# Kernel optimization log

Measured on AMD Instinct MI355X. Metric: run time of the kernel, lower is better.

Reference implementation:

```python
import jax, jax.numpy as jnp
import numpy as np

IN_FEATURES = 256
EMBED = 512
HEADS = 8
HEAD_DIM = EMBED // HEADS
BLOCKS = 2
FFN = 2048
CLASSES = 1000
NWIRES = 8
BATCH = 8
SEQ = 2048


def _posenc(seq, dim, dtype):
    pos = jnp.arange(seq, dtype=jnp.float32)[:, None]
    div = jnp.exp(jnp.arange(0, dim, 2, dtype=jnp.float32) * (-jnp.log(10000.0) / dim))
    pe = jnp.zeros((seq, dim), dtype=jnp.float32)
    pe = pe.at[:, 0::2].set(jnp.sin(pos * div))
    pe = pe.at[:, 1::2].set(jnp.cos(pos * div))
    return pe.astype(dtype)


def _layer_norm(x, g, b, eps=1e-5):
    mu = jnp.mean(x, axis=-1, keepdims=True)
    var = jnp.var(x, axis=-1, keepdims=True)
    return (x - mu) * jax.lax.rsqrt(var + eps) * g + b


def setup_inputs() -> dict:
    key = jax.random.key(0)
    ks = jax.random.split(key, 20)
    s = 0.02
    inp = {
        'x': jax.random.normal(ks[0], (BATCH, SEQ, IN_FEATURES), dtype=jnp.float32),
        'Wi': jax.random.normal(ks[1], (EMBED, IN_FEATURES), dtype=jnp.float32) * s,
        'bi': jnp.zeros((EMBED,), dtype=jnp.float32),
        'theta_a': jax.random.normal(ks[2], (BLOCKS, NWIRES), dtype=jnp.float32),
        'Wproj': jax.random.normal(ks[3], (BLOCKS, EMBED, NWIRES), dtype=jnp.float32) * s,
        'Wq': jax.random.normal(ks[4], (BLOCKS, EMBED, EMBED), dtype=jnp.float32) * s,
        'Wk': jax.random.normal(ks[5], (BLOCKS, EMBED, EMBED), dtype=jnp.float32) * s,
        'Wv': jax.random.normal(ks[6], (BLOCKS, EMBED, EMBED), dtype=jnp.float32) * s,
        'Wo': jax.random.normal(ks[7], (BLOCKS, EMBED, EMBED), dtype=jnp.float32) * s,
        'g1': jnp.ones((BLOCKS, EMBED), dtype=jnp.float32),
        'b1': jnp.zeros((BLOCKS, EMBED), dtype=jnp.float32),
        'phi': jax.random.normal(ks[8], (BLOCKS, NWIRES), dtype=jnp.float32),
        'W1': jax.random.normal(ks[9], (BLOCKS, FFN, NWIRES), dtype=jnp.float32) * s,
        'W2': jax.random.normal(ks[10], (BLOCKS, EMBED, FFN), dtype=jnp.float32) * s,
        'g2': jnp.ones((BLOCKS, EMBED), dtype=jnp.float32),
        'b2': jnp.zeros((BLOCKS, EMBED), dtype=jnp.float32),
        'Wc': jax.random.normal(ks[11], (CLASSES, EMBED), dtype=jnp.float32) * s,
        'bc': jnp.zeros((CLASSES,), dtype=jnp.float32),
    }
    return inp


def reference(x, Wi, bi, theta_a, Wproj, Wq, Wk, Wv, Wo, g1, b1, phi, W1, W2, g2, b2, Wc, bc):
    b, s, _ = x.shape
    h = jnp.einsum('bsf,ef->bse', x, Wi) + bi          # input_proj
    h = h + _posenc(s, EMBED, h.dtype)[None]           # positional encoding
    scale = 1.0 / np.sqrt(HEAD_DIM)
    for l in range(BLOCKS):
        # --- quantum attention sublayer ---
        # RX encode first NWIRES features + trainable RX per wire -> <Z> = cos(x + theta)
        q_out = jnp.cos(h[..., :NWIRES] + theta_a[l])  # [b,s,nw]
        x_q = jnp.einsum('bsw,ew->bse', q_out, Wproj[l])
        q = jnp.einsum('bse,fe->bsf', x_q, Wq[l]).reshape(b, s, HEADS, HEAD_DIM).transpose(0, 2, 1, 3)
        k = jnp.einsum('bse,fe->bsf', x_q, Wk[l]).reshape(b, s, HEADS, HEAD_DIM).transpose(0, 2, 1, 3)
        v = jnp.einsum('bse,fe->bsf', x_q, Wv[l]).reshape(b, s, HEADS, HEAD_DIM).transpose(0, 2, 1, 3)
        scores = jnp.einsum('bhqd,bhkd->bhqk', q, k) * scale
        attn = jax.nn.softmax(scores, axis=-1)
        out = jnp.einsum('bhqk,bhkd->bhqd', attn, v)
        out = out.transpose(0, 2, 1, 3).reshape(b, s, EMBED)
        attn_out = jnp.einsum('bse,fe->bsf', out, Wo[l])
        h = _layer_norm(h + attn_out, g1[l], b1[l])
        # --- quantum feed-forward sublayer ---
        # RY encode + trainable RY per wire -> <Z> = cos(x + phi)
        qf = jnp.cos(h[..., :NWIRES] + phi[l])         # [b,s,nw]
        f = jnp.einsum('bsw,fw->bsf', qf, W1[l])       # nw -> ffn
        f = jnp.einsum('bsf,ef->bse', jax.nn.relu(f), W2[l])
        h = _layer_norm(h + f, g2[l], b2[l])
    pooled = jnp.mean(h, axis=1)                        # [b, embed]
    logits = jnp.einsum('be,ce->bc', pooled, Wc) + bc
    return logits
```

## Files before the change

kernel.cpp:

```cpp
#include <hip/hip_runtime.h>
#include <hip/hip_bf16.h>
#include <math.h>

#define B_   8
#define S_   2048
#define T_   (B_*S_)
#define FIN  256
#define E_   512
#define H_   8
#define D_   64
#define FFN_ 2048
#define NC_  1000
#define NW_  8

typedef __attribute__((ext_vector_type(8))) short short8;
typedef __attribute__((ext_vector_type(4))) short short4v;
typedef __attribute__((ext_vector_type(4))) float f32x4;
typedef __attribute__((ext_vector_type(2))) unsigned int uint2v;
typedef __attribute__((ext_vector_type(4))) unsigned int uint4v;

__device__ __forceinline__ unsigned short f2bf(float f) {
    __hip_bfloat16 h = __float2bfloat16(f);
    return __builtin_bit_cast(unsigned short, h);
}
__device__ __forceinline__ float bf2f(unsigned short u) {
    return __builtin_bit_cast(float, (unsigned int)u << 16);
}

__device__ __forceinline__ unsigned cvtpk_bf16(float lo, float hi) {
    unsigned r;
    asm("v_cvt_pk_bf16_f32 %0, %1, %2" : "=v"(r) : "v"(lo), "v"(hi));
    return r;
}

#if defined(__has_builtin)
#if __has_builtin(__builtin_amdgcn_permlane32_swap) && __has_builtin(__builtin_amdgcn_permlane16_swap)
#define HAVE_PLSWAP 1
#endif
#endif

__device__ __forceinline__ void lswap32(unsigned &a, unsigned &b) {
#if defined(HAVE_PLSWAP)
    uint2v t = __builtin_amdgcn_permlane32_swap(a, b, false, false);
    a = t[0]; b = t[1];
#else
    unsigned as = (unsigned)__shfl_xor((int)a, 32);
    unsigned bs = (unsigned)__shfl_xor((int)b, 32);
    bool hi = (threadIdx.x & 32) != 0;
    unsigned na = hi ? bs : a;
    unsigned nb = hi ? b  : as;
    a = na; b = nb;
#endif
}
__device__ __forceinline__ void lswap16(unsigned &a, unsigned &b) {
#if defined(HAVE_PLSWAP)
    uint2v t = __builtin_amdgcn_permlane16_swap(a, b, false, false);
    a = t[0]; b = t[1];
#else
    unsigned as = (unsigned)__shfl_xor((int)a, 16);
    unsigned bs = (unsigned)__shfl_xor((int)b, 16);
    bool hi = (threadIdx.x & 16) != 0;
    unsigned na = hi ? bs : a;
    unsigned nb = hi ? b  : as;
    a = na; b = nb;
#endif
}

__device__ __forceinline__ void gld16(void* l, const void* g) {
    __builtin_amdgcn_global_load_lds(
        (const __attribute__((address_space(1))) unsigned int*)g,
        (__attribute__((address_space(3))) unsigned int*)l,
        16, 0, 0);
}

#if defined(__has_builtin)
#if __has_builtin(__builtin_amdgcn_mfma_f32_16x16x16bf16_1k)
#define HAVE_MFMA16 1
#endif
#endif

__device__ __forceinline__ f32x4 mfma16(short4v a, short4v b, f32x4 c) {
#ifdef HAVE_MFMA16
    return __builtin_amdgcn_mfma_f32_16x16x16bf16_1k(a, b, c, 0, 0, 0);
#else
    short8 a8 = {a[0], a[1], a[2], a[3], 0, 0, 0, 0};
    short8 b8 = {b[0], b[1], b[2], b[3], 0, 0, 0, 0};
    return __builtin_amdgcn_mfma_f32_16x16x32_bf16(a8, b8, c, 0, 0, 0);
#endif
}

__global__ __launch_bounds__(256)
void cvt_all(const float* __restrict__ x,  const float* __restrict__ Wi,
             const float* __restrict__ Wo, const float* __restrict__ W2,
             const float* __restrict__ W1,
             unsigned short* xb, unsigned short* Wib,
             unsigned short* Wob, unsigned short* W2b, unsigned short* W1b)
{
    int g = blockIdx.x*256 + threadIdx.x;
    const float* s; unsigned short* d; int o;
    if      (g < 1048576) { s = x;  d = xb;  o = g; }
    else if (g < 1081344) { s = Wi; d = Wib; o = g - 1048576; }
    else if (g < 1212416) { s = Wo; d = Wob; o = g - 1081344; }
    else if (g < 1736704) { s = W2; d = W2b; o = g - 1212416; }
    else                  { s = W1; d = W1b; o = g - 1736704; }
    float4 vv = ((const float4*)s)[o];
    ushort4 u;
    u.x = f2bf(vv.x); u.y = f2bf(vv.y); u.z = f2bf(vv.z); u.w = f2bf(vv.w);
    ((ushort4*)d)[o] = u;
}

__global__ __launch_bounds__(64)
void weff_kernel(const float* __restrict__ Wq, const float* __restrict__ Wk,
                 const float* __restrict__ Wv, const float* __restrict__ Wproj,
                 unsigned short* __restrict__ Weff)
{
    const int f = blockIdx.x, l = blockIdx.y, which = blockIdx.z;
    const int lane = threadIdx.x;
    const float* W = (which == 0 ? Wq : which == 1 ? Wk : Wv)
                     + (size_t)l*E_*E_ + (size_t)f*E_;
    const float* P = Wproj + (size_t)l*E_*NW_;
    const int wv = lane & 7;
    float s = 0.f;
    for (int e = (lane >> 3)*64; e < (lane >> 3)*64 + 64; e++)
        s += W[e] * P[e*NW_ + wv];
    #pragma unroll
    for (int off = 8; off < 64; off <<= 1) s += __shfl_xor(s, off);
    const float scale = (which == 0) ? 0.18033688011112042f : 1.f;
    if (lane < 8)
        Weff[((size_t)(which*2 + l)*E_ + f)*NW_ + lane] = f2bf(s * scale);
}

__global__ __launch_bounds__(256)
void qkv_small(const unsigned short* __restrict__ h, const float* __restrict__ theta,
               const unsigned short* __restrict__ Wq_e,
               const unsigned short* __restrict__ Wk_e,
               const unsigned short* __restrict__ Wv_e,
               unsigned short* __restrict__ qo, unsigned short* __restrict__ ko,
               unsigned short* __restrict__ vT)
{
    const int tid = threadIdx.x;
    const int t0 = blockIdx.x * 32;
    __shared__ float cs[32][8];
    {
        int tl = tid >> 3, wv2 = tid & 7;
        cs[tl][wv2] = cosf(bf2f(h[(size_t)(t0 + tl)*E_ + wv2]) + theta[wv2]);
    }
    __syncthreads();
    const int f = tid * 2;
    float wq[16], wk[16], wv_[16];
    #pragma unroll
    for (int i = 0; i < 16; i++) {
        wq[i]  = bf2f(Wq_e[(size_t)f*NW_ + i]);
        wk[i]  = bf2f(Wk_e[(size_t)f*NW_ + i]);
        wv_[i] = bf2f(Wv_e[(size_t)f*NW_ + i]);
    }
    unsigned int v0p[16] __attribute__((aligned(16)));
    unsigned int v1p[16] __attribute__((aligned(16)));
    for (int t = 0; t < 32; t++) {
        float4 c01 = *(const float4*)&cs[t][0];
        float4 c23 = *(const float4*)&cs[t][4];
        float c[8] = {c01.x,c01.y,c01.z,c01.w,c23.x,c23.y,c23.z,c23.w};
        float q0=0,q1=0,k0=0,k1=0,v0=0,v1=0;
        #pragma unroll
        for (int i = 0; i < 8; i++) {
            q0 += c[i]*wq[i];  q1 += c[i]*wq[8+i];
            k0 += c[i]*wk[i];  k1 += c[i]*wk[8+i];
            v0 += c[i]*wv_[i]; v1 += c[i]*wv_[8+i];
        }
        size_t base = (size_t)(t0 + t)*E_ + f;
        ushort2 uq; uq.x = f2bf(q0); uq.y = f2bf(q1);
        ushort2 uk; uk.x = f2bf(k0); uk.y = f2bf(k1);
        *(ushort2*)&qo[base] = uq;
        *(ushort2*)&ko[base] = uk;
        unsigned int b0 = f2bf(v0), b1 = f2bf(v1);
        if (t & 1) { v0p[t>>1] |= b0 << 16; v1p[t>>1] |= b1 << 16; }
        else       { v0p[t>>1]  = b0;       v1p[t>>1]  = b1; }
    }
    const int bb = t0 >> 11, s0 = t0 & (S_ - 1);
    const int head = f >> 6, d = f & 63;
    unsigned short* r0 = vT + ((size_t)(bb*H_ + head)*64 + d)*S_ + s0;
    #pragma unroll
    for (int c = 0; c < 4; c++) *(float4*)(r0 + c*8) = *(float4*)&v0p[c*4];
    r0 += S_;
    #pragma unroll
    for (int c = 0; c < 4; c++) *(float4*)(r0 + c*8) = *(float4*)&v1p[c*4];
}

template<int TC_BF16, int MODE>
__global__ __launch_bounds__(256)
void gemm_mfma(const unsigned short* __restrict__ A,
               const unsigned short* __restrict__ Bm,
               void* __restrict__ Cv, int M, int N, int K,
               float scale, const float* __restrict__ bias)
{
    __shared__ char Lraw[32768];
    unsigned short* Al = (unsigned short*)Lraw;
    unsigned short* Bl = (unsigned short*)(Lraw + 16384);
    float* Ot = (float*)Lraw;

    const int tid  = threadIdx.x;
    const int lane = tid & 63;
    const int w    = tid >> 6;
    const int wx   = w & 1, wy = w >> 1;
    int bx, by;
    {
        int nx = gridDim.x;
        int bid = blockIdx.y * nx + blockIdx.x;
        int rpx = gridDim.y >> 3;
        int xcd = bid & 7, idx = bid >> 3;
        by = xcd * rpx + idx / nx;
        bx = idx % nx;
    }
    const int rowBase = by * 128;
    const int colBase = bx * 128;
    const int l15  = lane & 15;
    const int quad = lane >> 4;
    const int srow = lane >> 2;
    const int gch  = (lane & 3) ^ ((srow >> 1) & 3);
    const int swz  = (l15 >> 1) & 3;

    f32x4 acc[4][4] = {};

    #pragma unroll
    for (int it = 0; it < 2; it++) {
        int rb = it*64 + w*16;
        gld16(&Al[rb*32], A  + (size_t)(rowBase + rb + srow)*K + gch*8);
        gld16(&Bl[rb*32], Bm + (size_t)(colBase + rb + srow)*K + gch*8);
    }

    for (int k0 = 0; k0 < K; k0 += 32) {
        const int cur = (k0 >> 5) & 1;
        __syncthreads();
        if (k0 + 32 < K) {
            #pragma unroll
            for (int it = 0; it < 2; it++) {
                int rb = it*64 + w*16;
                gld16(&Al[(1-cur)*4096 + rb*32], A  + (size_t)(rowBase + rb + srow)*K + k0 + 32 + gch*8);
                gld16(&Bl[(1-cur)*4096 + rb*32], Bm + (size_t)(colBase + rb + srow)*K + k0 + 32 + gch*8);
            }
        }
        short8 af[4], bfr[4];
        #pragma unroll
        for (int mi = 0; mi < 4; mi++)
            af[mi] = *(const short8*)&Al[cur*4096 + (wy*64 + mi*16 + l15)*32 + ((quad ^ swz) << 3)];
        #pragma unroll
        for (int ni = 0; ni < 4; ni++)
            bfr[ni] = *(const short8*)&Bl[cur*4096 + (wx*64 + ni*16 + l15)*32 + ((quad ^ swz) << 3)];
        #pragma unroll
        for (int mi = 0; mi < 4; mi++)
            #pragma unroll
            for (int ni = 0; ni < 4; ni++)
                acc[mi][ni] = __builtin_amdgcn_mfma_f32_16x16x32_bf16(
                    af[mi], bfr[ni], acc[mi][ni], 0, 0, 0);
    }

    #pragma unroll
    for (int mi = 0; mi < 4; mi++) {
        __syncthreads();
        #pragma unroll
        for (int ni = 0; ni < 4; ni++) {
            #pragma unroll
            for (int r = 0; r < 4; r++) {
                float v = acc[mi][ni][r] * scale;
                if (MODE == 1) {
                    int row = rowBase + wy*64 + mi*16 + quad*4 + r;
                    int col = colBase + wx*64 + ni*16 + l15;
                    int s = row & (S_ - 1);
                    float freq = __expf(-0.017988946039244957f * (float)(col & ~1));
                    float ang = (float)s * freq;
                    v += bias[col] + ((col & 1) ? cosf(ang) : sinf(ang));
                }
                Ot[(wy*16 + quad*4 + r)*132 + wx*64 + ni*16 + l15] = v;
            }
        }
        __syncthreads();
        {
            int rl = tid >> 3, c0 = (tid & 7) * 16;
            int grow = rowBase + (rl >> 4)*64 + mi*16 + (rl & 15);
            float vv[16];
            #pragma unroll
            for (int j = 0; j < 4; j++)
                *(float4*)&vv[j*4] = *(const float4*)&Ot[rl*132 + c0 + j*4];
            if (TC_BF16) {
                unsigned short u[16] __attribute__((aligned(16)));
                #pragma unroll
                for (int i = 0; i < 16; i++) u[i] = f2bf(vv[i]);
                unsigned short* dst = (unsigned short*)Cv + (size_t)grow*N + colBase + c0;
                *(float4*)dst       = *(float4*)&u[0];
                *(float4*)(dst + 8) = *(float4*)&u[8];
            } else {
                float* dst = (float*)Cv + (size_t)grow*N + colBase + c0;
                #pragma unroll
                for (int j = 0; j < 4; j++)
                    *(float4*)(dst + j*4) = *(const float4*)&vv[j*4];
            }
        }
    }
}

__global__ __launch_bounds__(256)
void gemm_w2f(const unsigned short* __restrict__ h, const float* __restrict__ phi,
              const unsigned short* __restrict__ W1b,
              const unsigned short* __restrict__ W2b,
              unsigned short* __restrict__ tmp)
{
    __shared__ char Lraw[17408];
    unsigned short* Wl = (unsigned short*)Lraw;
    float* Ot = (float*)Lraw;

    const int tid  = threadIdx.x;
    const int lane = tid & 63;
    const int w    = tid >> 6;
    const int tx   = w & 1, ty = w >> 1;
    const int l15  = lane & 15;
    const int quad = lane >> 4;
    const int srow = lane >> 2;
    const int gch  = (lane & 3) ^ ((srow >> 1) & 3);
    const int swz  = (l15 >> 1) & 3;

    const int bid = blockIdx.x;
    const int xcd = bid & 7;
    const int eb  = xcd >> 1;
    const int tb  = (xcd & 1) * 64 + (bid >> 3);
    const int tBase = tb * 128;
    const int eBase = eb * 128;

    short4v cosfr[4];
    #pragma unroll
    for (int nt = 0; nt < 4; nt++) {
        short4v c = {0,0,0,0};
        if (quad < 2) {
            int tok = tBase + ty*64 + nt*16 + l15;
            #pragma unroll
            for (int i = 0; i < 4; i++) {
                int wv = quad*4 + i;
                c[i] = (short)f2bf(cosf(bf2f(h[(size_t)tok*E_ + wv]) + phi[wv]));
            }
        }
        cosfr[nt] = c;
    }

    #pragma unroll
    for (int it = 0; it < 2; it++) {
        int rb = w*32 + it*16;
        gld16(&Wl[rb*32], W2b + (size_t)(eBase + rb + srow)*FFN_ + gch*8);
    }
    short4v w1f[2] = {{0,0,0,0},{0,0,0,0}};
    #pragma unroll
    for (int jb = 0; jb < 2; jb++)
        if (quad < 2)
            w1f[jb] = *(const short4v*)&W1b[(size_t)(jb*16 + l15)*NW_ + quad*4];

    f32x4 acc[4][4] = {};
    const f32x4 fzero = {0.f, 0.f, 0.f, 0.f};

    for (int k0 = 0; k0 < FFN_; k0 += 32) {
        const int cur = (k0 >> 5) & 1;
        __syncthreads();
        if (k0 + 32 < FFN_) {
            #pragma unroll
            for (int it = 0; it < 2; it++) {
                int rb = w*32 + it*16;
                gld16(&Wl[(1-cur)*4096 + rb*32],
                      W2b + (size_t)(eBase + rb + srow)*FFN_ + k0 + 32 + gch*8);
            }
        }
        unsigned Pm[4][4];
        #pragma unroll
        for (int nt = 0; nt < 4; nt++) {
            #pragma unroll
            for (int jb = 0; jb < 2; jb++) {
                f32x4 c = mfma16(w1f[jb], cosfr[nt], fzero);
                Pm[nt][jb*2]   = cvtpk_bf16(fmaxf(c[0], 0.f), fmaxf(c[1], 0.f));
                Pm[nt][jb*2+1] = cvtpk_bf16(fmaxf(c[2], 0.f), fmaxf(c[3], 0.f));
            }
            lswap32(Pm[nt][0], Pm[nt][2]); lswap32(Pm[nt][1], Pm[nt][3]);
            lswap16(Pm[nt][0], Pm[nt][2]); lswap16(Pm[nt][1], Pm[nt][3]);
        }
        short8 pfr[4];
        #pragma unroll
        for (int nt = 0; nt < 4; nt++) {
            uint4v u = { Pm[nt][0], Pm[nt][1], Pm[nt][2], Pm[nt][3] };
            pfr[nt] = __builtin_bit_cast(short8, u);
        }
        if (k0 + 32 < FFN_) {
            #pragma unroll
            for (int jb = 0; jb < 2; jb++)
                if (quad < 2)
                    w1f[jb] = *(const short4v*)&W1b[(size_t)(k0 + 32 + jb*16 + l15)*NW_ + quad*4];
        }
        #pragma unroll
        for (int et = 0; et < 4; et++) {
            short8 wf = *(const short8*)&Wl[cur*4096 + (tx*64 + et*16 + l15)*32
                                             + ((quad ^ swz) << 3)];
            #pragma unroll
            for (int nt = 0; nt < 4; nt++)
                acc[et][nt] = __builtin_amdgcn_mfma_f32_16x16x32_bf16(
                    wf, pfr[nt], acc[et][nt], 0, 0, 0);
        }
    }

    #pragma unroll
    for (int et = 0; et < 4; et++) {
        __syncthreads();
        #pragma unroll
        for (int nt = 0; nt < 4; nt++)
            #pragma unroll
            for (int r = 0; r < 4; r++)
                Ot[(ty*64 + nt*16 + l15)*33 + tx*16 + quad*4 + r] = acc[et][nt][r];
        __syncthreads();
        int token = tid >> 1, half = tid & 1;
        unsigned short u[16] __attribute__((aligned(16)));
        #pragma unroll
        for (int i = 0; i < 16; i++) u[i] = f2bf(Ot[token*33 + half*16 + i]);
        unsigned short* dst = tmp + (size_t)(tBase + token)*E_ + eBase + half*64 + et*16;
        *(float4*)dst       = *(float4*)&u[0];
        *(float4*)(dst + 8) = *(float4*)&u[8];
    }
}

__global__ __launch_bounds__(256)
void flash_attn(const unsigned short* __restrict__ q,
                const unsigned short* __restrict__ k,
                const unsigned short* __restrict__ vT,
                unsigned short* __restrict__ o)
{
    __shared__ unsigned short L[17168];
    unsigned short* Ks = L;
    unsigned short* Vt = L + 8192;
    float* Ot = (float*)L;

    const int tid  = threadIdx.x;
    const int lane = tid & 63;
    const int w    = tid >> 6;
    const int l15  = lane & 15;
    const int quad = lane >> 4;
    const int bid  = blockIdx.x;
    const int xcd  = bid & 7;
    const int rest = bid >> 3;
    const int combo = xcd * 8 + (rest >> 4);
    const int qt = rest & 15;
    const int hh = combo & 7;
    const int bb = combo >> 3;
    const size_t qrow0 = (size_t)bb*S_ + (size_t)qt*128;
    const unsigned short* qp  = q  + qrow0*E_ + hh*64;
    const unsigned short* kp  = k  + ((size_t)bb*S_)*E_ + hh*64;
    const unsigned short* vtp = vT + (size_t)(bb*H_ + hh)*64*S_;

    const int srow8 = lane >> 3;
    const int gch8  = (lane & 7) ^ srow8;
    const int sql   = l15 & 7;

    #pragma unroll
    for (int it = 0; it < 4; it++) {
        int rb = it*32 + w*8;
        gld16(&L[rb*64], qp + (size_t)(rb + srow8)*E_ + gch8*8);
    }
    __syncthreads();
    short8 qfr[2][2];
    #pragma unroll
    for (int mi = 0; mi < 2; mi++)
        #pragma unroll
        for (int kc = 0; kc < 2; kc++)
            qfr[mi][kc] = *(const short8*)&L[(w*32 + mi*16 + l15)*64
                                             + (((kc*4 + quad) ^ sql) << 3)];
    __syncthreads();

    #pragma unroll
    for (int it = 0; it < 2; it++) {
        int rb = it*32 + w*8;
        gld16(&Ks[rb*64], kp  + (size_t)(rb + srow8)*E_ + gch8*8);
        gld16(&Vt[rb*64], vtp + (size_t)(rb + srow8)*S_ + gch8*8);
    }

    const short8 ones8 = {(short)0x3F80, (short)0x3F80, (short)0x3F80, (short)0x3F80,
                          (short)0x3F80, (short)0x3F80, (short)0x3F80, (short)0x3F80};
    f32x4 O[2][4] = {};
    f32x4 Ol[2]   = {};

    for (int kt = 0; kt < S_/64; kt++) {
        const int cur = kt & 1;
        __syncthreads();
        if (kt + 1 < S_/64) {
            #pragma unroll
            for (int it = 0; it < 2; it++) {
                int rb = it*32 + w*8;
                gld16(&Ks[(1-cur)*4096 + rb*64],
                      kp  + (size_t)((kt+1)*64 + rb + srow8)*E_ + gch8*8);
                gld16(&Vt[(1-cur)*4096 + rb*64],
                      vtp + (size_t)(rb + srow8)*S_ + (kt+1)*64 + gch8*8);
            }
        }
        f32x4 Sc[2][4] = {};
        #pragma unroll
        for (int kc = 0; kc < 2; kc++)
            #pragma unroll
            for (int nt = 0; nt < 4; nt++) {
                short8 kf = *(const short8*)&Ks[cur*4096 + (nt*16 + l15)*64
                                                 + (((kc*4 + quad) ^ sql) << 3)];
                Sc[0][nt] = __builtin_amdgcn_mfma_f32_16x16x32_bf16(kf, qfr[0][kc], Sc[0][nt], 0, 0, 0);
                Sc[1][nt] = __builtin_amdgcn_mfma_f32_16x16x32_bf16(kf, qfr[1][kc], Sc[1][nt], 0, 0, 0);
            }
        unsigned Pm[2][8];
        #pragma unroll
        for (int mi = 0; mi < 2; mi++)
            #pragma unroll
            for (int nt = 0; nt < 4; nt++) {
                float e0 = __builtin_amdgcn_exp2f(Sc[mi][nt][0]);
                float e1 = __builtin_amdgcn_exp2f(Sc[mi][nt][1]);
                float e2 = __builtin_amdgcn_exp2f(Sc[mi][nt][2]);
                float e3 = __builtin_amdgcn_exp2f(Sc[mi][nt][3]);
                Pm[mi][nt*2]   = cvtpk_bf16(e0, e1);
                Pm[mi][nt*2+1] = cvtpk_bf16(e2, e3);
            }
        #pragma unroll
        for (int mi = 0; mi < 2; mi++) {
            lswap32(Pm[mi][0], Pm[mi][2]); lswap32(Pm[mi][1], Pm[mi][3]);
            lswap32(Pm[mi][4], Pm[mi][6]); lswap32(Pm[mi][5], Pm[mi][7]);
            lswap16(Pm[mi][0], Pm[mi][2]); lswap16(Pm[mi][1], Pm[mi][3]);
            lswap16(Pm[mi][4], Pm[mi][6]); lswap16(Pm[mi][5], Pm[mi][7]);
        }
        short8 pf[2][2];
        #pragma unroll
        for (int mi = 0; mi < 2; mi++)
            #pragma unroll
            for (int kb = 0; kb < 2; kb++) {
                uint4v u = { Pm[mi][kb*4], Pm[mi][kb*4+1], Pm[mi][kb*4+2], Pm[mi][kb*4+3] };
                pf[mi][kb] = __builtin_bit_cast(short8, u);
                Ol[mi] = __builtin_amdgcn_mfma_f32_16x16x32_bf16(ones8, pf[mi][kb], Ol[mi], 0, 0, 0);
            }
        #pragma unroll
        for (int dt = 0; dt < 4; dt++)
            #pragma unroll
            for (int kb = 0; kb < 2; kb++) {
                short8 vf = *(const short8*)&Vt[cur*4096 + (dt*16 + l15)*64
                                                 + (((kb*4 + quad) ^ sql) << 3)];
                O[0][dt] = __builtin_amdgcn_mfma_f32_16x16x32_bf16(vf, pf[0][kb], O[0][dt], 0, 0, 0);
                O[1][dt] = __builtin_amdgcn_mfma_f32_16x16x32_bf16(vf, pf[1][kb], O[1][dt], 0, 0, 0);
            }
    }

    __syncthreads();
    #pragma unroll
    for (int mi = 0; mi < 2; mi++) {
        float inv = 1.f / Ol[mi][0];
        #pragma unroll
        for (int dt = 0; dt < 4; dt++)
            #pragma unroll
            for (int r = 0; r < 4; r++)
                Ot[(w*32 + mi*16 + l15)*67 + dt*16 + quad*4 + r] = O[mi][dt][r] * inv;
    }
    __syncthreads();
    {
        int row = tid >> 1, half = tid & 1;
        unsigned short u[32] __attribute__((aligned(16)));
        #pragma unroll
        for (int i = 0; i < 32; i++) u[i] = f2bf(Ot[row*67 + half*32 + i]);
        unsigned short* dst = o + (qrow0 + row)*E_ + hh*64 + half*32;
        #pragma unroll
        for (int c = 0; c < 4; c++) *(float4*)(dst + c*8) = *(float4*)&u[c*8];
    }
}

__global__ __launch_bounds__(256)
void add_ln(unsigned short* __restrict__ h, const unsigned short* __restrict__ delta,
            const float* __restrict__ g, const float* __restrict__ b)
{
    const int lane = threadIdx.x & 63;
    const int t = blockIdx.x*4 + (threadIdx.x >> 6);
    const size_t base = (size_t)t*E_ + lane*8;
    uint4 hv = *(const uint4*)&h[base];
    uint4 dv = *(const uint4*)&delta[base];
    float x[8];
    #pragma unroll
    for (int i = 0; i < 4; i++) {
        unsigned hu = ((const unsigned*)&hv)[i], du = ((const unsigned*)&dv)[i];
        x[2*i]   = bf2f((unsigned short)(hu & 0xffff)) + bf2f((unsigned short)(du & 0xffff));
        x[2*i+1] = bf2f((unsigned short)(hu >> 16))    + bf2f((unsigned short)(du >> 16));
    }
    float s = 0.f, sq = 0.f;
    #pragma unroll
    for (int i = 0; i < 8; i++) { s += x[i]; sq += x[i]*x[i]; }
    #pragma unroll
    for (int off = 1; off < 64; off <<= 1) {
        s  += __shfl_xor(s,  off);
        sq += __shfl_xor(sq, off);
    }
    float mu  = s * (1.f/E_);
    float var = sq * (1.f/E_) - mu*mu;
    float rstd = rsqrtf(var + 1e-5f);
    float4 g0 = *(const float4*)&g[lane*8], g1 = *(const float4*)&g[lane*8 + 4];
    float4 b0 = *(const float4*)&b[lane*8], b1 = *(const float4*)&b[lane*8 + 4];
    float gg[8] = {g0.x,g0.y,g0.z,g0.w,g1.x,g1.y,g1.z,g1.w};
    float bb[8] = {b0.x,b0.y,b0.z,b0.w,b1.x,b1.y,b1.z,b1.w};
    uint4 ov;
    #pragma unroll
    for (int i = 0; i < 4; i++) {
        unsigned lo = f2bf((x[2*i]   - mu)*rstd*gg[2*i]   + bb[2*i]);
        unsigned hi = f2bf((x[2*i+1] - mu)*rstd*gg[2*i+1] + bb[2*i+1]);
        ((unsigned*)&ov)[i] = lo | (hi << 16);
    }
    *(uint4*)&h[base] = ov;
}

__global__ __launch_bounds__(256)
void pool_partial(const unsigned short* __restrict__ h, float* __restrict__ part)
{
    const int chunk = blockIdx.x, bb = blockIdx.y, tid = threadIdx.x;
    for (int e = tid; e < E_; e += 256) {
        const unsigned short* p = h + ((size_t)bb*S_ + (size_t)chunk*128)*E_ + e;
        float s = 0.f;
        for (int r = 0; r < 128; r++) s += bf2f(p[(size_t)r*E_]);
        part[(size_t)(bb*16 + chunk)*E_ + e] = s;
    }
}

__global__ __launch_bounds__(256)
void pool_final(const float* __restrict__ part, float* __restrict__ pooled)
{
    const int bb = blockIdx.x, tid = threadIdx.x;
    for (int e = tid; e < E_; e += 256) {
        float s = 0.f;
        #pragma unroll
        for (int c = 0; c < 16; c++) s += part[(size_t)(bb*16 + c)*E_ + e];
        pooled[bb*E_ + e] = s * (1.f/S_);
    }
}

__global__ __launch_bounds__(64)
void classify(const float* __restrict__ pooled, const float* __restrict__ Wc,
              const float* __restrict__ bc, float* __restrict__ out)
{
    const int c = blockIdx.x, bb = blockIdx.y, lane = threadIdx.x;
    const float* p = pooled + bb*E_;
    const float* wc = Wc + (size_t)c*E_;
    float s = 0.f;
    for (int e = lane; e < E_; e += 64) s += p[e]*wc[e];
    #pragma unroll
    for (int off = 1; off < 64; off <<= 1) s += __shfl_xor(s, off);
    if (lane == 0) out[bb*NC_ + c] = s + bc[c];
}

extern "C" void kernel_launch(void* const* d_in, const int* in_sizes, int n_in,
                              void* d_out, int out_size, void* d_ws, size_t ws_size,
                              hipStream_t stream)
{
    const float* x       = (const float*)d_in[0];
    const float* Wi      = (const float*)d_in[1];
    const float* bi      = (const float*)d_in[2];
    const float* theta_a = (const float*)d_in[3];
    const float* Wproj   = (const float*)d_in[4];
    const float* Wq      = (const float*)d_in[5];
    const float* Wk      = (const float*)d_in[6];
    const float* Wv      = (const float*)d_in[7];
    const float* Wo      = (const float*)d_in[8];
    const float* g1      = (const float*)d_in[9];
    const float* b1      = (const float*)d_in[10];
    const float* phi     = (const float*)d_in[11];
    const float* W1      = (const float*)d_in[12];
    const float* W2      = (const float*)d_in[13];
    const float* g2      = (const float*)d_in[14];
    const float* b2      = (const float*)d_in[15];
    const float* Wc      = (const float*)d_in[16];
    const float* bc      = (const float*)d_in[17];
    float* out = (float*)d_out;

    char* ws = (char*)d_ws;
    const size_t MB = 1024u*1024u;
    unsigned short* h      = (unsigned short*)(ws + 0*MB);
    unsigned short* tmp    = (unsigned short*)(ws + 16*MB);
    unsigned short* qb     = (unsigned short*)(ws + 32*MB);
    unsigned short* kb     = (unsigned short*)(ws + 48*MB);
    unsigned short* vT     = (unsigned short*)(ws + 64*MB);
    unsigned short* ao     = (unsigned short*)(ws + 80*MB);
    unsigned short* xb     = (unsigned short*)(ws + 96*MB);
    unsigned short* Wib    = (unsigned short*)(ws + 104*MB);
    unsigned short* Wob    = (unsigned short*)(ws + 105*MB);
    unsigned short* W2b    = (unsigned short*)(ws + 106*MB);
    unsigned short* W1b    = (unsigned short*)(ws + 110*MB);
    unsigned short* Weff   = (unsigned short*)(ws + 111*MB);
    float*          part   = (float*)(ws + 112*MB);
    float*          pooled = (float*)(ws + 112*MB + 512*1024);

    cvt_all<<<6816, 256, 0, stream>>>(x, Wi, Wo, W2, W1, xb, Wib, Wob, W2b, W1b);
    weff_kernel<<<dim3(E_, 2, 3), 64, 0, stream>>>(Wq, Wk, Wv, Wproj, Weff);

    gemm_mfma<1,1><<<dim3(E_/128, T_/128), 256, 0, stream>>>(
        xb, Wib, h, T_, E_, FIN, 1.f, bi);

    for (int l = 0; l < 2; l++) {
        const unsigned short* Wq_e = Weff + (size_t)(0*2 + l)*E_*NW_;
        const unsigned short* Wk_e = Weff + (size_t)(1*2 + l)*E_*NW_;
        const unsigned short* Wv_e = Weff + (size_t)(2*2 + l)*E_*NW_;
        qkv_small<<<T_/32, 256, 0, stream>>>(h, theta_a + l*NW_, Wq_e, Wk_e, Wv_e, qb, kb, vT);
        flash_attn<<<(S_/128)*H_*B_, 256, 0, stream>>>(qb, kb, vT, ao);
        gemm_mfma<1,0><<<dim3(E_/128, T_/128), 256, 0, stream>>>(
            ao, Wob + (size_t)l*E_*E_, tmp, T_, E_, E_, 1.f, nullptr);
        add_ln<<<T_/4, 256, 0, stream>>>(h, tmp, g1 + l*E_, b1 + l*E_);

        gemm_w2f<<<512, 256, 0, stream>>>(h, phi + l*NW_,
                                          W1b + (size_t)l*FFN_*NW_,
                                          W2b + (size_t)l*E_*FFN_, tmp);
        add_ln<<<T_/4, 256, 0, stream>>>(h, tmp, g2 + l*E_, b2 + l*E_);
    }

    pool_partial<<<dim3(16, B_), 256, 0, stream>>>(h, part);
    pool_final<<<B_, 256, 0, stream>>>(part, pooled);
    classify<<<dim3(NC_, B_), 64, 0, stream>>>(pooled, Wc, bc, out);
}
```

Baseline: 638.6 us.

## Exploit rank-8 structure: attention scores via Gram matrix, fold Wv into Wo

```diff
diff --git a/kernel.cpp b/kernel.cpp
--- a/kernel.cpp
+++ b/kernel.cpp
@@ -130,60 +130,80 @@
         Weff[((size_t)(which*2 + l)*E_ + f)*NW_ + lane] = f2bf(s * scale);
 }
 
-__global__ __launch_bounds__(256)
-void qkv_small(const unsigned short* __restrict__ h, const float* __restrict__ theta,
-               const unsigned short* __restrict__ Wq_e,
-               const unsigned short* __restrict__ Wk_e,
-               const unsigned short* __restrict__ Wv_e,
-               unsigned short* __restrict__ qo, unsigned short* __restrict__ ko,
-               unsigned short* __restrict__ vT)
+__global__ __launch_bounds__(64)
+void gram_kernel(const unsigned short* __restrict__ Weff, unsigned short* __restrict__ G)
+{
+    const int hh = blockIdx.x, l = blockIdx.y;
+    const int lane = threadIdx.x;
+    const int w = lane >> 3, wp = lane & 7;
+    const unsigned short* Wq_e = Weff + (size_t)(0*2 + l)*E_*NW_ + (size_t)hh*64*NW_;
+    const unsigned short* Wk_e = Weff + (size_t)(1*2 + l)*E_*NW_ + (size_t)hh*64*NW_;
+    float s = 0.f;
+    for (int d = 0; d < 64; d++)
+        s += bf2f(Wq_e[d*NW_ + w]) * bf2f(Wk_e[d*NW_ + wp]);
+    G[(size_t)(l*8 + hh)*64 + w*8 + wp] = f2bf(s);
+}
+
+__global__ __launch_bounds__(64)
+void wov_kernel(const float* __restrict__ Wo, const unsigned short* __restrict__ Weff,
+                unsigned short* __restrict__ WoV)
+{
+    const int f = blockIdx.x, l = blockIdx.y;
+    const int lane = threadIdx.x;
+    const int hh = lane >> 3, w = lane & 7;
+    const float* wrow = Wo + (size_t)l*E_*E_ + (size_t)f*E_ + hh*64;
+    const unsigned short* Wv_e = Weff + (size_t)(2*2 + l)*E_*NW_ + (size_t)hh*64*NW_;
+    float s = 0.f;
+    for (int d = 0; d < 64; d++)
+        s += wrow[d] * bf2f(Wv_e[d*NW_ + w]);
+    WoV[(size_t)(l*E_ + f)*64 + lane] = f2bf(s);
+}
+
+__global__ __launch_bounds__(256)
+void qc_small(const unsigned short* __restrict__ h, const float* __restrict__ theta,
+              const unsigned short* __restrict__ G,
+              unsigned short* __restrict__ c8, unsigned short* __restrict__ c8T,
+              unsigned short* __restrict__ gkb)
 {
     const int tid = threadIdx.x;
     const int t0 = blockIdx.x * 32;
     __shared__ float cs[32][8];
+    __shared__ float Gs[512];
     {
         int tl = tid >> 3, wv2 = tid & 7;
         cs[tl][wv2] = cosf(bf2f(h[(size_t)(t0 + tl)*E_ + wv2]) + theta[wv2]);
+        Gs[tid]       = bf2f(G[tid]);
+        Gs[tid + 256] = bf2f(G[tid + 256]);
     }
     __syncthreads();
-    const int f = tid * 2;
-    float wq[16], wk[16], wv_[16];
-    #pragma unroll
-    for (int i = 0; i < 16; i++) {
-        wq[i]  = bf2f(Wq_e[(size_t)f*NW_ + i]);
-        wk[i]  = bf2f(Wk_e[(size_t)f*NW_ + i]);
-        wv_[i] = bf2f(Wv_e[(size_t)f*NW_ + i]);
-    }
-    unsigned int v0p[16] __attribute__((aligned(16)));
-    unsigned int v1p[16] __attribute__((aligned(16)));
-    for (int t = 0; t < 32; t++) {
-        float4 c01 = *(const float4*)&cs[t][0];
-        float4 c23 = *(const float4*)&cs[t][4];
-        float c[8] = {c01.x,c01.y,c01.z,c01.w,c23.x,c23.y,c23.z,c23.w};
-        float q0=0,q1=0,k0=0,k1=0,v0=0,v1=0;
-        #pragma unroll
-        for (int i = 0; i < 8; i++) {
-            q0 += c[i]*wq[i];  q1 += c[i]*wq[8+i];
-            k0 += c[i]*wk[i];  k1 += c[i]*wk[8+i];
-            v0 += c[i]*wv_[i]; v1 += c[i]*wv_[8+i];
-        }
-        size_t base = (size_t)(t0 + t)*E_ + f;
-        ushort2 uq; uq.x = f2bf(q0); uq.y = f2bf(q1);
-        ushort2 uk; uk.x = f2bf(k0); uk.y = f2bf(k1);
-        *(ushort2*)&qo[base] = uq;
-        *(ushort2*)&ko[base] = uk;
-        unsigned int b0 = f2bf(v0), b1 = f2bf(v1);
-        if (t & 1) { v0p[t>>1] |= b0 << 16; v1p[t>>1] |= b1 << 16; }
-        else       { v0p[t>>1]  = b0;       v1p[t>>1]  = b1; }
-    }
-    const int bb = t0 >> 11, s0 = t0 & (S_ - 1);
-    const int head = f >> 6, d = f & 63;
-    unsigned short* r0 = vT + ((size_t)(bb*H_ + head)*64 + d)*S_ + s0;
-    #pragma unroll
-    for (int c = 0; c < 4; c++) *(float4*)(r0 + c*8) = *(float4*)&v0p[c*4];
-    r0 += S_;
-    #pragma unroll
-    for (int c = 0; c < 4; c++) *(float4*)(r0 + c*8) = *(float4*)&v1p[c*4];
+    const int tl = tid >> 3, hh = tid & 7;
+    const int bb = (t0 + tl) >> 11, ss = (t0 + tl) & (S_ - 1);
+    float c[8];
+    #pragma unroll
+    for (int i = 0; i < 8; i++) c[i] = cs[tl][i];
+    unsigned short u[8] __attribute__((aligned(16)));
+    #pragma unroll
+    for (int w = 0; w < 8; w++) {
+        float s = 0.f;
+        #pragma unroll
+        for (int wp = 0; wp < 8; wp++) s += Gs[hh*64 + w*8 + wp] * c[wp];
+        u[w] = f2bf(s);
+    }
+    *(float4*)&gkb[((size_t)(bb*H_ + hh)*S_ + ss)*8] = *(float4*)u;
+    if (tid < 32) {
+        unsigned short v[8] __attribute__((aligned(16)));
+        #pragma unroll
+        for (int i = 0; i < 8; i++) v[i] = f2bf(cs[tid][i]);
+        *(float4*)&c8[(size_t)(t0 + tid)*8] = *(float4*)v;
+    } else if (tid < 40) {
+        int w = tid - 32;
+        unsigned short v[32] __attribute__((aligned(16)));
+        #pragma unroll
+        for (int s = 0; s < 32; s++) v[s] = f2bf(cs[s][w]);
+        unsigned short* dst = c8T + ((size_t)(t0 >> 11)*8 + w)*S_ + (t0 & (S_ - 1));
+        #pragma unroll
+        for (int cq = 0; cq < 4; cq++) *(float4*)(dst + cq*8) = *(float4*)&v[cq*8];
+    }
 }
 
 template<int TC_BF16, int MODE>
@@ -420,19 +440,14 @@
 }
 
 __global__ __launch_bounds__(256)
-void flash_attn(const unsigned short* __restrict__ q,
-                const unsigned short* __restrict__ k,
-                const unsigned short* __restrict__ vT,
-                unsigned short* __restrict__ o)
-{
-    __shared__ unsigned short L[17168];
-    unsigned short* Ks = L;
-    unsigned short* Vt = L + 8192;
-    float* Ot = (float*)L;
-
+void flash_q(const unsigned short* __restrict__ c8,
+             const unsigned short* __restrict__ c8T,
+             const unsigned short* __restrict__ gkb,
+             unsigned short* __restrict__ yout)
+{
     const int tid  = threadIdx.x;
     const int lane = tid & 63;
-    const int w    = tid >> 6;
+    const int wv   = tid >> 6;
     const int l15  = lane & 15;
     const int quad = lane >> 4;
     const int bid  = blockIdx.x;
@@ -443,64 +458,29 @@
     const int hh = combo & 7;
     const int bb = combo >> 3;
     const size_t qrow0 = (size_t)bb*S_ + (size_t)qt*128;
-    const unsigned short* qp  = q  + qrow0*E_ + hh*64;
-    const unsigned short* kp  = k  + ((size_t)bb*S_)*E_ + hh*64;
-    const unsigned short* vtp = vT + (size_t)(bb*H_ + hh)*64*S_;
-
-    const int srow8 = lane >> 3;
-    const int gch8  = (lane & 7) ^ srow8;
-    const int sql   = l15 & 7;
-
-    #pragma unroll
-    for (int it = 0; it < 4; it++) {
-        int rb = it*32 + w*8;
-        gld16(&L[rb*64], qp + (size_t)(rb + srow8)*E_ + gch8*8);
-    }
-    __syncthreads();
-    short8 qfr[2][2];
-    #pragma unroll
-    for (int mi = 0; mi < 2; mi++)
-        #pragma unroll
-        for (int kc = 0; kc < 2; kc++)
-            qfr[mi][kc] = *(const short8*)&L[(w*32 + mi*16 + l15)*64
-                                             + (((kc*4 + quad) ^ sql) << 3)];
-    __syncthreads();
-
-    #pragma unroll
-    for (int it = 0; it < 2; it++) {
-        int rb = it*32 + w*8;
-        gld16(&Ks[rb*64], kp  + (size_t)(rb + srow8)*E_ + gch8*8);
-        gld16(&Vt[rb*64], vtp + (size_t)(rb + srow8)*S_ + gch8*8);
-    }
-
+    const unsigned short* gkp  = gkb + (size_t)(bb*H_ + hh)*S_*NW_;
+    const unsigned short* c8Tp = c8T + (size_t)bb*8*S_;
+
+    short4v cqfr[2] = {{0,0,0,0},{0,0,0,0}};
+    if (quad < 2) {
+        #pragma unroll
+        for (int mi = 0; mi < 2; mi++)
+            cqfr[mi] = *(const short4v*)&c8[(qrow0 + wv*32 + mi*16 + l15)*NW_ + quad*4];
+    }
     const short8 ones8 = {(short)0x3F80, (short)0x3F80, (short)0x3F80, (short)0x3F80,
                           (short)0x3F80, (short)0x3F80, (short)0x3F80, (short)0x3F80};
-    f32x4 O[2][4] = {};
-    f32x4 Ol[2]   = {};
+    f32x4 y[2] = {};
 
     for (int kt = 0; kt < S_/64; kt++) {
-        const int cur = kt & 1;
-        __syncthreads();
-        if (kt + 1 < S_/64) {
-            #pragma unroll
-            for (int it = 0; it < 2; it++) {
-                int rb = it*32 + w*8;
-                gld16(&Ks[(1-cur)*4096 + rb*64],
-                      kp  + (size_t)((kt+1)*64 + rb + srow8)*E_ + gch8*8);
-                gld16(&Vt[(1-cur)*4096 + rb*64],
-                      vtp + (size_t)(rb + srow8)*S_ + (kt+1)*64 + gch8*8);
-            }
-        }
         f32x4 Sc[2][4] = {};
         #pragma unroll
-        for (int kc = 0; kc < 2; kc++)
-            #pragma unroll
-            for (int nt = 0; nt < 4; nt++) {
-                short8 kf = *(const short8*)&Ks[cur*4096 + (nt*16 + l15)*64
-                                                 + (((kc*4 + quad) ^ sql) << 3)];
-                Sc[0][nt] = __builtin_amdgcn_mfma_f32_16x16x32_bf16(kf, qfr[0][kc], Sc[0][nt], 0, 0, 0);
-                Sc[1][nt] = __builtin_amdgcn_mfma_f32_16x16x32_bf16(kf, qfr[1][kc], Sc[1][nt], 0, 0, 0);
-            }
+        for (int nt = 0; nt < 4; nt++) {
+            short4v gkf = {0,0,0,0};
+            if (quad < 2)
+                gkf = *(const short4v*)&gkp[(size_t)(kt*64 + nt*16 + l15)*NW_ + quad*4];
+            Sc[0][nt] = mfma16(gkf, cqfr[0], Sc[0][nt]);
+            Sc[1][nt] = mfma16(gkf, cqfr[1], Sc[1][nt]);
+        }
         unsigned Pm[2][8];
         #pragma unroll
         for (int mi = 0; mi < 2; mi++)
@@ -527,38 +507,29 @@
             for (int kb = 0; kb < 2; kb++) {
                 uint4v u = { Pm[mi][kb*4], Pm[mi][kb*4+1], Pm[mi][kb*4+2], Pm[mi][kb*4+3] };
                 pf[mi][kb] = __builtin_bit_cast(short8, u);
-                Ol[mi] = __builtin_amdgcn_mfma_f32_16x16x32_bf16(ones8, pf[mi][kb], Ol[mi], 0, 0, 0);
-            }
-        #pragma unroll
-        for (int dt = 0; dt < 4; dt++)
-            #pragma unroll
-            for (int kb = 0; kb < 2; kb++) {
-                short8 vf = *(const short8*)&Vt[cur*4096 + (dt*16 + l15)*64
-                                                 + (((kb*4 + quad) ^ sql) << 3)];
-                O[0][dt] = __builtin_amdgcn_mfma_f32_16x16x32_bf16(vf, pf[0][kb], O[0][dt], 0, 0, 0);
-                O[1][dt] = __builtin_amdgcn_mfma_f32_16x16x32_bf16(vf, pf[1][kb], O[1][dt], 0, 0, 0);
-            }
-    }
-
-    __syncthreads();
+            }
+        #pragma unroll
+        for (int kb = 0; kb < 2; kb++) {
+            short8 a8 = {0,0,0,0,0,0,0,0};
+            if (l15 < 8)
+                a8 = *(const short8*)&c8Tp[(size_t)l15*S_ + kt*64 + kb*32 + quad*8];
+            else if (l15 == 8)
+                a8 = ones8;
+            y[0] = __builtin_amdgcn_mfma_f32_16x16x32_bf16(a8, pf[0][kb], y[0], 0, 0, 0);
+            y[1] = __builtin_amdgcn_mfma_f32_16x16x32_bf16(a8, pf[1][kb], y[1], 0, 0, 0);
+        }
+    }
+
     #pragma unroll
     for (int mi = 0; mi < 2; mi++) {
-        float inv = 1.f / Ol[mi][0];
-        #pragma unroll
-        for (int dt = 0; dt < 4; dt++)
-            #pragma unroll
-            for (int r = 0; r < 4; r++)
-                Ot[(w*32 + mi*16 + l15)*67 + dt*16 + quad*4 + r] = O[mi][dt][r] * inv;
-    }
-    __syncthreads();
-    {
-        int row = tid >> 1, half = tid & 1;
-        unsigned short u[32] __attribute__((aligned(16)));
-        #pragma unroll
-        for (int i = 0; i < 32; i++) u[i] = f2bf(Ot[row*67 + half*32 + i]);
-        unsigned short* dst = o + (qrow0 + row)*E_ + hh*64 + half*32;
-        #pragma unroll
-        for (int c = 0; c < 4; c++) *(float4*)(dst + c*8) = *(float4*)&u[c*8];
+        float rs = __shfl(y[mi][0], 32 + l15);
+        float inv = 1.f / rs;
+        if (quad < 2) {
+            unsigned d0 = cvtpk_bf16(y[mi][0]*inv, y[mi][1]*inv);
+            unsigned d1 = cvtpk_bf16(y[mi][2]*inv, y[mi][3]*inv);
+            unsigned* dst = (unsigned*)&yout[(qrow0 + wv*32 + mi*16 + l15)*64 + hh*8 + quad*4];
+            dst[0] = d0; dst[1] = d1;
+        }
     }
 }
 
@@ -669,33 +640,35 @@
     const size_t MB = 1024u*1024u;
     unsigned short* h      = (unsigned short*)(ws + 0*MB);
     unsigned short* tmp    = (unsigned short*)(ws + 16*MB);
-    unsigned short* qb     = (unsigned short*)(ws + 32*MB);
-    unsigned short* kb     = (unsigned short*)(ws + 48*MB);
-    unsigned short* vT     = (unsigned short*)(ws + 64*MB);
-    unsigned short* ao     = (unsigned short*)(ws + 80*MB);
+    unsigned short* c8     = (unsigned short*)(ws + 32*MB);
+    unsigned short* c8T    = (unsigned short*)(ws + 33*MB);
+    unsigned short* gkb    = (unsigned short*)(ws + 34*MB);
+    unsigned short* yout   = (unsigned short*)(ws + 48*MB);
     unsigned short* xb     = (unsigned short*)(ws + 96*MB);
     unsigned short* Wib    = (unsigned short*)(ws + 104*MB);
     unsigned short* Wob    = (unsigned short*)(ws + 105*MB);
     unsigned short* W2b    = (unsigned short*)(ws + 106*MB);
     unsigned short* W1b    = (unsigned short*)(ws + 110*MB);
     unsigned short* Weff   = (unsigned short*)(ws + 111*MB);
+    unsigned short* Gbuf   = (unsigned short*)(ws + 111*MB + 64*1024);
+    unsigned short* WoV    = (unsigned short*)(ws + 111*MB + 128*1024);
     float*          part   = (float*)(ws + 112*MB);
     float*          pooled = (float*)(ws + 112*MB + 512*1024);
 
     cvt_all<<<6816, 256, 0, stream>>>(x, Wi, Wo, W2, W1, xb, Wib, Wob, W2b, W1b);
     weff_kernel<<<dim3(E_, 2, 3), 64, 0, stream>>>(Wq, Wk, Wv, Wproj, Weff);
+    gram_kernel<<<dim3(H_, 2), 64, 0, stream>>>(Weff, Gbuf);
+    wov_kernel<<<dim3(E_, 2), 64, 0, stream>>>(Wo, Weff, WoV);
 
     gemm_mfma<1,1><<<dim3(E_/128, T_/128), 256, 0, stream>>>(
         xb, Wib, h, T_, E_, FIN, 1.f, bi);
 
     for (int l = 0; l < 2; l++) {
-        const unsigned short* Wq_e = Weff + (size_t)(0*2 + l)*E_*NW_;
-        const unsigned short* Wk_e = Weff + (size_t)(1*2 + l)*E_*NW_;
-        const unsigned short* Wv_e = Weff + (size_t)(2*2 + l)*E_*NW_;
-        qkv_small<<<T_/32, 256, 0, stream>>>(h, theta_a + l*NW_, Wq_e, Wk_e, Wv_e, qb, kb, vT);
-        flash_attn<<<(S_/128)*H_*B_, 256, 0, stream>>>(qb, kb, vT, ao);
+        qc_small<<<T_/32, 256, 0, stream>>>(h, theta_a + l*NW_, Gbuf + (size_t)l*512,
+                                            c8, c8T, gkb);
+        flash_q<<<(S_/128)*H_*B_, 256, 0, stream>>>(c8, c8T, gkb, yout);
         gemm_mfma<1,0><<<dim3(E_/128, T_/128), 256, 0, stream>>>(
-            ao, Wob + (size_t)l*E_*E_, tmp, T_, E_, E_, 1.f, nullptr);
+            yout, WoV + (size_t)l*E_*64, tmp, T_, E_, 64, 1.f, nullptr);
         add_ln<<<T_/4, 256, 0, stream>>>(h, tmp, g1 + l*E_, b1 + l*E_);
 
         gemm_w2f<<<512, 256, 0, stream>>>(h, phi + l*NW_,
```

New measurement: 580.4 us. 1.1x faster.
